# Kernel optimization log

Measured on AMD Instinct MI355X. Metric: run time of the kernel, lower is better.

Reference implementation:

```python
import jax, jax.numpy as jnp
import numpy as np
import math

H = 16
SEG = 128
DIL = 2


def hilbert_perm(M: int) -> jnp.ndarray:
    # Boustrophedon (snake) traversal of a ceil(sqrt(M)) grid, matching
    # create_hilbert_mapping_simple: skip linear positions >= M, keep first M.
    g = int(math.ceil(math.sqrt(M)))
    grid = np.arange(g * g).reshape(g, g)
    grid[1::2] = grid[1::2, ::-1]
    flat = grid.reshape(-1)
    flat = flat[flat < M][:M]
    return jnp.asarray(flat, dtype=jnp.int32)


def setup_inputs() -> dict:
    key = jax.random.key(0)
    kx, kq, ko = jax.random.split(key, 3)
    B, M, D = 4, 4096, 1024
    x = jax.random.normal(kx, (B, M, D), dtype=jnp.float32)
    # nn.Linear weights: [out_features, in_features], y = x @ W.T
    w_qkv = jax.random.normal(kq, (3 * D, D), dtype=jnp.float32) * (D ** -0.5)
    w_out = jax.random.normal(ko, (D, D), dtype=jnp.float32) * (D ** -0.5)
    return {"x": x, "w_qkv": w_qkv, "w_out": w_out}


def reference(x, w_qkv, w_out):
    B, M, Dm = x.shape
    hd = Dm // H
    scale = hd ** -0.5
    S = M // SEG  # number of segments (M chosen as a multiple of SEG)

    qkv = x @ w_qkv.T                              # [B, M, 3*Dm]
    qkv = qkv.reshape(B, M, 3, H, hd)
    q = qkv[:, :, 0].transpose(0, 2, 1, 3)         # [B, H, M, hd]
    k = qkv[:, :, 1].transpose(0, 2, 1, 3)
    v = qkv[:, :, 2].transpose(0, 2, 1, 3)

    perm = hilbert_perm(M)
    qh = q[:, :, perm]                             # Hilbert-reordered
    kh = k[:, :, perm]
    vh = v[:, :, perm]

    # segment-local dilated attention: each query attends to keys at
    # positions seg_start + j*DIL within its own segment
    qh = qh.reshape(B, H, S, SEG, hd)
    kd = kh.reshape(B, H, S, SEG, hd)[:, :, :, ::DIL]   # [B,H,S,SEG//DIL,hd]
    vd = vh.reshape(B, H, S, SEG, hd)[:, :, :, ::DIL]

    scores = jnp.einsum('bhsqd,bhskd->bhsqk', qh * scale, kd)
    attn = jax.nn.softmax(scores, axis=-1)
    o = jnp.einsum('bhsqk,bhskd->bhsqd', attn, vd)       # [B,H,S,SEG,hd]
    o = o.reshape(B, H, M, hd).transpose(0, 2, 1, 3).reshape(B, M, Dm)
    return o @ w_out.T
```

## Files before the change

### kernel.cpp

```cpp
#include <hip/hip_runtime.h>


typedef _Float16 f16x8 __attribute__((ext_vector_type(8)));
typedef _Float16 f16x4 __attribute__((ext_vector_type(4)));
typedef float f32x4 __attribute__((ext_vector_type(4)));

__device__ __forceinline__ int hperm(int i) {
  int r = i >> 6, c = i & 63;
  return (r << 6) | ((r & 1) ? (63 - c) : c);
}

__device__ __forceinline__ int arow_gather(int mp) {
  int b = mp >> 11, i = mp & 2047;
  int s = i >> 6, j = i & 63;
  return b * 4096 + hperm(s * 128 + 2 * j);
}

__device__ __forceinline__ void gload_lds16(const _Float16* g, _Float16* l) {
  __builtin_amdgcn_global_load_lds(
      (const __attribute__((address_space(1))) void*)g,
      (__attribute__((address_space(3))) void*)l, 16, 0, 0);
}

__global__ __launch_bounds__(256) void cast_all(
    const float* __restrict__ x, _Float16* __restrict__ xh,
    const float* __restrict__ wq, _Float16* __restrict__ wqh,
    const float* __restrict__ wo, _Float16* __restrict__ woh) {
  int i = blockIdx.x * 256 + threadIdx.x;
  const float* s;
  _Float16* d;
  int j;
  if (i < 4194304) {
    s = x; d = xh; j = i;
  } else if (i < 4194304 + 786432) {
    s = wq; d = wqh; j = i - 4194304;
  } else {
    s = wo; d = woh; j = i - (4194304 + 786432);
  }
  float4 v = ((const float4*)s)[j];
  f16x4 o;
  o[0] = (_Float16)v.x;
  o[1] = (_Float16)v.y;
  o[2] = (_Float16)v.z;
  o[3] = (_Float16)v.w;
  *(f16x4*)&d[(size_t)j * 4] = o;
}


#define BAR __builtin_amdgcn_s_barrier()
#define LGKM0                                          \
  do {                                                 \
    asm volatile("s_waitcnt lgkmcnt(0)" ::: "memory"); \
    __builtin_amdgcn_sched_barrier(0);                 \
  } while (0)
#define VM4 asm volatile("s_waitcnt vmcnt(4)" ::: "memory")
#define VM0 asm volatile("s_waitcnt vmcnt(0)" ::: "memory")

#define STG(mat, kt, h, buf)                                               \
  do {                                                                     \
    const _Float16* g0 = ((mat) ? gpB : gpA)[(h)*2] + (size_t)(kt)*64;     \
    const _Float16* g1 = ((mat) ? gpB : gpA)[(h)*2 + 1] + (size_t)(kt)*64; \
    _Float16* d_ = &lds[buf][mat][h][t * 8];                               \
    gload_lds16(g0, d_);                                                   \
    gload_lds16(g1, d_ + 4096);                                            \
  } while (0)

#define LDA_(buf, mh)                                             \
  _Pragma("unroll") for (int m = 0; m < 4; m++) {                 \
    a[0][m] = *(const f16x8*)(aB[buf][0] + (mh)*4096 + m * 1024); \
    a[1][m] = *(const f16x8*)(aB[buf][1] + (mh)*4096 + m * 1024); \
  }

#define LDB_(buf, nh)                                                   \
  _Pragma("unroll") for (int nf = 0; nf < 2; nf++) {                    \
    b[nh][0][nf] = *(const f16x8*)(bB[buf][0] + (nh)*2048 + nf * 1024); \
    b[nh][1][nf] = *(const f16x8*)(bB[buf][1] + (nh)*2048 + nf * 1024); \
  }

#define MM_(mh, nh)                                                        \
  __builtin_amdgcn_s_setprio(1);                                           \
  _Pragma("unroll") for (int m = 0; m < 4; m++)                            \
      _Pragma("unroll") for (int nf = 0; nf < 2; nf++)                     \
          _Pragma("unroll") for (int ks = 0; ks < 2; ks++) acc[(mh)*4 + m] \
              [(nh)*2 + nf] = __builtin_amdgcn_mfma_f32_16x16x32_f16(      \
                  a[ks][m], b[nh][ks][nf], acc[(mh)*4 + m][(nh)*2 + nf],   \
                  0, 0, 0);                                                \
  __builtin_amdgcn_s_setprio(0);

template <typename OutT>
__device__ __forceinline__ void gemm_body(
    const _Float16* const* gpA, const _Float16* const* gpB,
    OutT* __restrict__ C, int N, size_t arow0, size_t brow0,
    _Float16 (&lds)[2][2][2][8192]) {
  const int t = threadIdx.x;
  const int lane = t & 63, wave = t >> 6;
  const int wm = wave >> 2, wn = wave & 3;
  const int lr = lane & 15, lg = lane >> 4;

  const int cx0 = (lg * 8) ^ ((lr & 7) << 3);
  const int cx1 = cx0 ^ 32;
  const _Float16* aB[2][2];
  const _Float16* bB[2][2];
#pragma unroll
  for (int bf = 0; bf < 2; bf++) {
    aB[bf][0] = &lds[bf][0][wm][lr * 64 + cx0];
    aB[bf][1] = &lds[bf][0][wm][lr * 64 + cx1];
    bB[bf][0] = &lds[bf][1][wn >> 1][(wn & 1) * 4096 + lr * 64 + cx0];
    bB[bf][1] = &lds[bf][1][wn >> 1][(wn & 1) * 4096 + lr * 64 + cx1];
  }

  f32x4 acc[8][4] = {};
  f16x8 a[2][4], b[2][2][2];

  STG(0, 0, 0, 0);
  STG(0, 0, 1, 0);
  STG(1, 0, 0, 0);
  STG(1, 0, 1, 0);
  STG(1, 1, 0, 1);
  STG(1, 1, 1, 1);
  VM4;
  BAR;

  for (int i = 0; i < 7; i++) {
    const int k1 = 2 * i + 1, k2 = 2 * i + 2, k3 = 2 * i + 3;
    LDA_(0, 0); LDB_(0, 0); STG(0, k1, 0, 1);      BAR; LGKM0; MM_(0, 0);
    LDB_(0, 1);             STG(0, k1, 1, 1);      BAR; LGKM0; MM_(0, 1);
    LDA_(0, 1);             STG(1, k2, 0, 0);      BAR; LGKM0; MM_(1, 1);
                            STG(1, k2, 1, 0); VM4; BAR; LGKM0; MM_(1, 0);
    LDA_(1, 0); LDB_(1, 0); STG(0, k2, 0, 0);      BAR; LGKM0; MM_(0, 0);
    LDB_(1, 1);             STG(0, k2, 1, 0);      BAR; LGKM0; MM_(0, 1);
    LDA_(1, 1);             STG(1, k3, 0, 1);      BAR; LGKM0; MM_(1, 1);
                            STG(1, k3, 1, 1); VM4; BAR; LGKM0; MM_(1, 0);
  }

  {
    LDA_(0, 0); LDB_(0, 0); STG(0, 15, 0, 1);      BAR; LGKM0; MM_(0, 0);
    LDB_(0, 1);             STG(0, 15, 1, 1);      BAR; LGKM0; MM_(0, 1);
    LDA_(0, 1);                                    BAR; LGKM0; MM_(1, 1);
                                              VM0; BAR; LGKM0; MM_(1, 0);
    LDA_(1, 0); LDB_(1, 0);                        BAR; LGKM0; MM_(0, 0);
    LDB_(1, 1);                                    BAR; LGKM0; MM_(0, 1);
    LDA_(1, 1);                                    BAR; LGKM0; MM_(1, 1);
                                                        LGKM0; MM_(1, 0);
  }

#pragma unroll
  for (int mf = 0; mf < 8; mf++) {
    size_t row0 = arow0 + wm * 128 + mf * 16 + lg * 4;
#pragma unroll
    for (int nf = 0; nf < 4; nf++) {
      size_t col = brow0 + wn * 64 + nf * 16 + lr;
#pragma unroll
      for (int j = 0; j < 4; j++)
        C[(row0 + j) * N + col] = (OutT)acc[mf][nf][j];
    }
  }
}

__global__ __launch_bounds__(512, 2) void gemm_qkv8(
    const _Float16* __restrict__ xh, const _Float16* __restrict__ wqh,
    _Float16* __restrict__ qh, _Float16* __restrict__ kvh) {
  __shared__ _Float16 lds[2][2][2][8192];
  const int t = threadIdx.x;
  const int id = blockIdx.x;
  const int sw = (id & 7) * (gridDim.x >> 3) + (id >> 3);
  const bool iskv = sw >= 256;
  const int wid = iskv ? sw - 256 : sw;
  const int N = iskv ? 2048 : 1024;
  const int bn = iskv ? (wid & 7) : (wid & 3);
  const int bm = iskv ? (wid >> 3) : (wid >> 2);
  const _Float16* Bw = wqh + (iskv ? (size_t)1048576 : 0);
  _Float16* C = iskv ? kvh : qh;

  const int sgrow = t >> 3;
  const int sgcol = ((t & 7) * 8) ^ ((sgrow & 7) << 3);
  const _Float16* gpA[4];
  const _Float16* gpB[4];
#pragma unroll
  for (int r = 0; r < 4; r++) {
    int mr = bm * 256 + 64 * r + sgrow;
    int ar = iskv ? arow_gather(mr) : mr;
    gpA[r] = xh + (size_t)ar * 1024 + sgcol;
    gpB[r] = Bw + ((size_t)bn * 256 + 64 * r + sgrow) * 1024 + sgcol;
  }
  gemm_body<_Float16>(gpA, gpB, C, N, (size_t)bm * 256, (size_t)bn * 256, lds);
}

__global__ __launch_bounds__(512, 2) void gemm_out8(
    const _Float16* __restrict__ atth, const _Float16* __restrict__ woh,
    float* __restrict__ out) {
  __shared__ _Float16 lds[2][2][2][8192];
  const int t = threadIdx.x;
  const int id = blockIdx.x;
  const int sw = (id & 7) * (gridDim.x >> 3) + (id >> 3);
  const int bn = sw & 3, bm = sw >> 2;

  const int sgrow = t >> 3;
  const int sgcol = ((t & 7) * 8) ^ ((sgrow & 7) << 3);
  const _Float16* gpA[4];
  const _Float16* gpB[4];
#pragma unroll
  for (int r = 0; r < 4; r++) {
    gpA[r] = atth + ((size_t)bm * 256 + 64 * r + sgrow) * 1024 + sgcol;
    gpB[r] = woh + ((size_t)bn * 256 + 64 * r + sgrow) * 1024 + sgcol;
  }
  gemm_body<float>(gpA, gpB, out, 1024, (size_t)bm * 256, (size_t)bn * 256,
                   lds);
}

#define STRD 72

__global__ __launch_bounds__(256) void hilbert_attn(
    const _Float16* __restrict__ qh, const _Float16* __restrict__ kvh,
    _Float16* __restrict__ aout) {
  __shared__ _Float16 Qs[128 * STRD];
  __shared__ _Float16 Ks[64 * STRD];
  __shared__ _Float16 Vt[64 * STRD];
  __shared__ _Float16 Ps[128 * STRD];
  const int blk = blockIdx.x;
  const int s = blk & 31, h = (blk >> 5) & 15, b = blk >> 9;
  const int t = threadIdx.x, lane = t & 63, wave = t >> 6;
  const int lr = lane & 15, lg = lane >> 4, lk = lg * 8;
  const int col = (t & 7) * 8, rr = t >> 3;
  const size_t kvb = ((size_t)b * 2048 + s * 64) * 2048;

#pragma unroll
  for (int i = 0; i < 4; i++) {
    int m = i * 32 + rr;
    int p = b * 4096 + hperm(s * 128 + m);
    *(f16x8*)&Qs[m * STRD + col] =
        *(const f16x8*)&qh[(size_t)p * 1024 + h * 64 + col];
  }
#pragma unroll
  for (int i = 0; i < 2; i++) {
    int j = i * 32 + rr;
    *(f16x8*)&Ks[j * STRD + col] =
        *(const f16x8*)&kvh[kvb + (size_t)j * 2048 + h * 64 + col];
    f16x8 vv =
        *(const f16x8*)&kvh[kvb + (size_t)j * 2048 + 1024 + h * 64 + col];
#pragma unroll
    for (int e = 0; e < 8; e++) Vt[(col + e) * STRD + j] = vv[e];
  }
  __syncthreads();

  f32x4 accs[2][4] = {};
#pragma unroll
  for (int kk = 0; kk < 2; kk++) {
    f16x8 aa[2], bb[4];
#pragma unroll
    for (int m = 0; m < 2; m++)
      aa[m] = *(const f16x8*)&Qs[(wave * 32 + m * 16 + lr) * STRD + kk * 32 + lk];
#pragma unroll
    for (int n = 0; n < 4; n++)
      bb[n] = *(const f16x8*)&Ks[(n * 16 + lr) * STRD + kk * 32 + lk];
#pragma unroll
    for (int m = 0; m < 2; m++)
#pragma unroll
      for (int n = 0; n < 4; n++)
        accs[m][n] =
            __builtin_amdgcn_mfma_f32_16x16x32_f16(aa[m], bb[n], accs[m][n], 0, 0, 0);
  }

#pragma unroll
  for (int m = 0; m < 2; m++) {
#pragma unroll
    for (int j = 0; j < 4; j++) {
      float sc0 = accs[m][0][j] * 0.125f;
      float sc1 = accs[m][1][j] * 0.125f;
      float sc2 = accs[m][2][j] * 0.125f;
      float sc3 = accs[m][3][j] * 0.125f;
      float mx = fmaxf(fmaxf(sc0, sc1), fmaxf(sc2, sc3));
#pragma unroll
      for (int d = 1; d < 16; d <<= 1) mx = fmaxf(mx, __shfl_xor(mx, d, 16));
      float e0 = __expf(sc0 - mx), e1 = __expf(sc1 - mx);
      float e2 = __expf(sc2 - mx), e3 = __expf(sc3 - mx);
      float sum = (e0 + e1) + (e2 + e3);
#pragma unroll
      for (int d = 1; d < 16; d <<= 1) sum += __shfl_xor(sum, d, 16);
      float inv = 1.0f / sum;
      int row = wave * 32 + m * 16 + lg * 4 + j;
      Ps[row * STRD + 0 * 16 + lr] = (_Float16)(e0 * inv);
      Ps[row * STRD + 1 * 16 + lr] = (_Float16)(e1 * inv);
      Ps[row * STRD + 2 * 16 + lr] = (_Float16)(e2 * inv);
      Ps[row * STRD + 3 * 16 + lr] = (_Float16)(e3 * inv);
    }
  }
  __syncthreads();

  f32x4 acco[2][4] = {};
#pragma unroll
  for (int kk = 0; kk < 2; kk++) {
    f16x8 aa[2], bb[4];
#pragma unroll
    for (int m = 0; m < 2; m++)
      aa[m] = *(const f16x8*)&Ps[(wave * 32 + m * 16 + lr) * STRD + kk * 32 + lk];
#pragma unroll
    for (int n = 0; n < 4; n++)
      bb[n] = *(const f16x8*)&Vt[(n * 16 + lr) * STRD + kk * 32 + lk];
#pragma unroll
    for (int m = 0; m < 2; m++)
#pragma unroll
      for (int n = 0; n < 4; n++)
        acco[m][n] =
            __builtin_amdgcn_mfma_f32_16x16x32_f16(aa[m], bb[n], acco[m][n], 0, 0, 0);
  }

  const size_t orow0 = (size_t)b * 4096 + s * 128;
#pragma unroll
  for (int m = 0; m < 2; m++) {
#pragma unroll
    for (int n = 0; n < 4; n++) {
#pragma unroll
      for (int j = 0; j < 4; j++) {
        size_t row = orow0 + wave * 32 + m * 16 + lg * 4 + j;
        aout[row * 1024 + h * 64 + n * 16 + lr] = (_Float16)acco[m][n][j];
      }
    }
  }
}

extern "C" void kernel_launch(void* const* d_in, const int* in_sizes, int n_in,
                              void* d_out, int out_size, void* d_ws, size_t ws_size,
                              hipStream_t stream) {
  const float* x = (const float*)d_in[0];
  const float* w_qkv = (const float*)d_in[1];
  const float* w_out = (const float*)d_in[2];
  float* out = (float*)d_out;
  char* ws = (char*)d_ws;

  _Float16* xh = (_Float16*)(ws + 0);
  _Float16* wqh = (_Float16*)(ws + (size_t)33554432);
  _Float16* woh = (_Float16*)(ws + (size_t)39845888);
  _Float16* qh = (_Float16*)(ws + (size_t)41943040);
  _Float16* kvh = (_Float16*)(ws + (size_t)75497472);
  _Float16* atth = (_Float16*)(ws + (size_t)109051904);

  cast_all<<<20480, 256, 0, stream>>>(x, xh, w_qkv, wqh, w_out, woh);

  gemm_qkv8<<<512, 512, 0, stream>>>(xh, wqh, qh, kvh);
  hilbert_attn<<<2048, 256, 0, stream>>>(qh, kvh, atth);
  gemm_out8<<<256, 512, 0, stream>>>(atth, woh, out);
}
```

Baseline: 158.4 us.

## Restructure GEMM main loop with 4x2 wave layout and register double-buffered A fragments

```diff
diff --git a/kernel.cpp b/kernel.cpp
--- a/kernel.cpp
+++ b/kernel.cpp
@@ -9,13 +9,11 @@
   int r = i >> 6, c = i & 63;
   return (r << 6) | ((r & 1) ? (63 - c) : c);
 }
-
 __device__ __forceinline__ int arow_gather(int mp) {
   int b = mp >> 11, i = mp & 2047;
   int s = i >> 6, j = i & 63;
   return b * 4096 + hperm(s * 128 + 2 * j);
 }
-
 __device__ __forceinline__ void gload_lds16(const _Float16* g, _Float16* l) {
   __builtin_amdgcn_global_load_lds(
       (const __attribute__((address_space(1))) void*)g,
@@ -26,141 +24,151 @@
     const float* __restrict__ x, _Float16* __restrict__ xh,
     const float* __restrict__ wq, _Float16* __restrict__ wqh,
     const float* __restrict__ wo, _Float16* __restrict__ woh) {
-  int i = blockIdx.x * 256 + threadIdx.x;
-  const float* s;
-  _Float16* d;
-  int j;
-  if (i < 4194304) {
-    s = x; d = xh; j = i;
-  } else if (i < 4194304 + 786432) {
-    s = wq; d = wqh; j = i - 4194304;
-  } else {
-    s = wo; d = woh; j = i - (4194304 + 786432);
-  }
-  float4 v = ((const float4*)s)[j];
-  f16x4 o;
-  o[0] = (_Float16)v.x;
-  o[1] = (_Float16)v.y;
-  o[2] = (_Float16)v.z;
-  o[3] = (_Float16)v.w;
-  *(f16x4*)&d[(size_t)j * 4] = o;
-}
-
+  for (int i = blockIdx.x * 256 + threadIdx.x; i < 5242880; i += 256 * 2048) {
+    const float* s;
+    _Float16* d;
+    int j;
+    if (i < 4194304) {
+      s = x; d = xh; j = i;
+    } else if (i < 4980736) {
+      s = wq; d = wqh; j = i - 4194304;
+    } else {
+      s = wo; d = woh; j = i - 4980736;
+    }
+    float4 v = ((const float4*)s)[j];
+    f16x4 o;
+    o[0] = (_Float16)v.x;
+    o[1] = (_Float16)v.y;
+    o[2] = (_Float16)v.z;
+    o[3] = (_Float16)v.w;
+    *(f16x4*)&d[(size_t)j * 4] = o;
+  }
+}
 
 #define BAR __builtin_amdgcn_s_barrier()
-#define LGKM0                                          \
-  do {                                                 \
-    asm volatile("s_waitcnt lgkmcnt(0)" ::: "memory"); \
-    __builtin_amdgcn_sched_barrier(0);                 \
+#define SB0 __builtin_amdgcn_sched_barrier(0)
+#define LGKM_(n)                                                  \
+  do {                                                            \
+    asm volatile("s_waitcnt lgkmcnt(" #n ")" ::: "memory");       \
+    SB0;                                                          \
   } while (0)
 #define VM4 asm volatile("s_waitcnt vmcnt(4)" ::: "memory")
+#define VM2 asm volatile("s_waitcnt vmcnt(2)" ::: "memory")
 #define VM0 asm volatile("s_waitcnt vmcnt(0)" ::: "memory")
-
-#define STG(mat, kt, h, buf)                                               \
-  do {                                                                     \
-    const _Float16* g0 = ((mat) ? gpB : gpA)[(h)*2] + (size_t)(kt)*64;     \
-    const _Float16* g1 = ((mat) ? gpB : gpA)[(h)*2 + 1] + (size_t)(kt)*64; \
-    _Float16* d_ = &lds[buf][mat][h][t * 8];                               \
-    gload_lds16(g0, d_);                                                   \
-    gload_lds16(g1, d_ + 4096);                                            \
+#define VMX
+
+#define RDA(dst, bi, ks)                                       \
+  _Pragma("unroll") for (int m = 0; m < 4; m++) dst[ks][m] =   \
+      *(const f16x8*)(aRd[bi][ks] + m * 1024);
+#define RDB(dst, bi, q)                                                     \
+  _Pragma("unroll") for (int ks = 0; ks < 2; ks++)                          \
+      _Pragma("unroll") for (int nf = 0; nf < 2; nf++) dst[ks][nf] =        \
+          *(const f16x8*)(bRd[bi][ks] + (q)*2048 + nf * 1024);
+
+#define SA(kt, buf, h)                                                        \
+  do {                                                                        \
+    gload_lds16(Ab + aOff[(h)*2] + (kt)*64, &lds[buf][0][(h)*8192 + t8]);     \
+    gload_lds16(Ab + aOff[(h)*2 + 1] + (kt)*64,                               \
+                &lds[buf][0][(h)*8192 + 4096 + t8]);                          \
   } while (0)
-
-#define LDA_(buf, mh)                                             \
-  _Pragma("unroll") for (int m = 0; m < 4; m++) {                 \
-    a[0][m] = *(const f16x8*)(aB[buf][0] + (mh)*4096 + m * 1024); \
-    a[1][m] = *(const f16x8*)(aB[buf][1] + (mh)*4096 + m * 1024); \
-  }
-
-#define LDB_(buf, nh)                                                   \
-  _Pragma("unroll") for (int nf = 0; nf < 2; nf++) {                    \
-    b[nh][0][nf] = *(const f16x8*)(bB[buf][0] + (nh)*2048 + nf * 1024); \
-    b[nh][1][nf] = *(const f16x8*)(bB[buf][1] + (nh)*2048 + nf * 1024); \
-  }
-
-#define MM_(mh, nh)                                                        \
-  __builtin_amdgcn_s_setprio(1);                                           \
-  _Pragma("unroll") for (int m = 0; m < 4; m++)                            \
-      _Pragma("unroll") for (int nf = 0; nf < 2; nf++)                     \
-          _Pragma("unroll") for (int ks = 0; ks < 2; ks++) acc[(mh)*4 + m] \
-              [(nh)*2 + nf] = __builtin_amdgcn_mfma_f32_16x16x32_f16(      \
-                  a[ks][m], b[nh][ks][nf], acc[(mh)*4 + m][(nh)*2 + nf],   \
-                  0, 0, 0);                                                \
+#define SBt(kt, buf, h)                                                       \
+  do {                                                                        \
+    gload_lds16(Bb + bOff[(h)*2] + (kt)*64, &lds[buf][1][(h)*8192 + t8]);     \
+    gload_lds16(Bb + bOff[(h)*2 + 1] + (kt)*64,                               \
+                &lds[buf][1][(h)*8192 + 4096 + t8]);                          \
+  } while (0)
+
+#define MMQ(AC, BS, q)                                                      \
+  __builtin_amdgcn_s_setprio(1);                                            \
+  _Pragma("unroll") for (int m = 0; m < 4; m++)                             \
+      _Pragma("unroll") for (int nf = 0; nf < 2; nf++)                      \
+          _Pragma("unroll") for (int ks = 0; ks < 2; ks++) acc[m][2 * (q) + \
+                                                               nf] =        \
+              __builtin_amdgcn_mfma_f32_16x16x32_f16(                       \
+                  AC[ks][m], BS[ks][nf], acc[m][2 * (q) + nf], 0, 0, 0);    \
   __builtin_amdgcn_s_setprio(0);
+
+#define KT(P, T, RD_A, S1, S2, S3, VQ2, VQ3, RD_B0, AN, AC, LGA, LGB3) \
+  do {                                                                 \
+                                                               \
+    if (RD_A) { RDA(AN, (P) ^ 1, 0); }                                 \
+    RDB(bS1, (P), 1);                                                  \
+    if (S1) { SBt((T) + 1, (P) ^ 1, 1); }                              \
+    BAR; LGKM_(LGA); MMQ(AC, bS0, 0);                                  \
+                                                               \
+    if (RD_A) { RDA(AN, (P) ^ 1, 1); }                                 \
+    RDB(bS0, (P), 2);                                                  \
+    if (S2) { SA((T) + 2, (P), 0); }                                   \
+    BAR; LGKM_(LGA); MMQ(AC, bS1, 1);                                  \
+                                                               \
+    RDB(bS1, (P), 3);                                                  \
+    if (S2) { SA((T) + 2, (P), 1); }                                   \
+    VQ2; BAR; LGKM_(4); MMQ(AC, bS0, 2);                               \
+                                                               \
+    if (RD_B0) { RDB(bS0, (P) ^ 1, 0); }                               \
+    if (S3) { SBt((T) + 2, (P), 0); }                                  \
+    VQ3; BAR; LGKM_(LGB3); MMQ(AC, bS1, 3);                            \
+  } while (0)
 
 template <typename OutT>
 __device__ __forceinline__ void gemm_body(
-    const _Float16* const* gpA, const _Float16* const* gpB,
-    OutT* __restrict__ C, int N, size_t arow0, size_t brow0,
-    _Float16 (&lds)[2][2][2][8192]) {
+    const _Float16* __restrict__ Ab, const _Float16* __restrict__ Bb,
+    const unsigned* aOff, const unsigned* bOff, OutT* __restrict__ C, int N,
+    size_t arow0, size_t bcol0, _Float16 (&lds)[2][2][16384]) {
   const int t = threadIdx.x;
   const int lane = t & 63, wave = t >> 6;
-  const int wm = wave >> 2, wn = wave & 3;
+  const int wm = wave >> 1, wn = wave & 1;
   const int lr = lane & 15, lg = lane >> 4;
+  const int t8 = t * 8;
 
   const int cx0 = (lg * 8) ^ ((lr & 7) << 3);
   const int cx1 = cx0 ^ 32;
-  const _Float16* aB[2][2];
-  const _Float16* bB[2][2];
+  const _Float16* aRd[2][2];
+  const _Float16* bRd[2][2];
 #pragma unroll
   for (int bf = 0; bf < 2; bf++) {
-    aB[bf][0] = &lds[bf][0][wm][lr * 64 + cx0];
-    aB[bf][1] = &lds[bf][0][wm][lr * 64 + cx1];
-    bB[bf][0] = &lds[bf][1][wn >> 1][(wn & 1) * 4096 + lr * 64 + cx0];
-    bB[bf][1] = &lds[bf][1][wn >> 1][(wn & 1) * 4096 + lr * 64 + cx1];
-  }
-
-  f32x4 acc[8][4] = {};
-  f16x8 a[2][4], b[2][2][2];
-
-  STG(0, 0, 0, 0);
-  STG(0, 0, 1, 0);
-  STG(1, 0, 0, 0);
-  STG(1, 0, 1, 0);
-  STG(1, 1, 0, 1);
-  STG(1, 1, 1, 1);
+    aRd[bf][0] = &lds[bf][0][(wm * 64 + lr) * 64 + cx0];
+    aRd[bf][1] = &lds[bf][0][(wm * 64 + lr) * 64 + cx1];
+    bRd[bf][0] = &lds[bf][1][(wn * 128 + lr) * 64 + cx0];
+    bRd[bf][1] = &lds[bf][1][(wn * 128 + lr) * 64 + cx1];
+  }
+
+  f32x4 acc[4][8] = {};
+  f16x8 aEv[2][4], aOd[2][4], bS0[2][2], bS1[2][2];
+
+  SA(0, 0, 0); SA(0, 0, 1); SBt(0, 0, 0); SBt(0, 0, 1);
+  SA(1, 1, 0); SA(1, 1, 1);
   VM4;
   BAR;
+  RDA(aEv, 0, 0); RDA(aEv, 0, 1); RDB(bS0, 0, 0);
+  SBt(1, 1, 0);
+  VM2;
+  BAR;
 
   for (int i = 0; i < 7; i++) {
-    const int k1 = 2 * i + 1, k2 = 2 * i + 2, k3 = 2 * i + 3;
-    LDA_(0, 0); LDB_(0, 0); STG(0, k1, 0, 1);      BAR; LGKM0; MM_(0, 0);
-    LDB_(0, 1);             STG(0, k1, 1, 1);      BAR; LGKM0; MM_(0, 1);
-    LDA_(0, 1);             STG(1, k2, 0, 0);      BAR; LGKM0; MM_(1, 1);
-                            STG(1, k2, 1, 0); VM4; BAR; LGKM0; MM_(1, 0);
-    LDA_(1, 0); LDB_(1, 0); STG(0, k2, 0, 0);      BAR; LGKM0; MM_(0, 0);
-    LDB_(1, 1);             STG(0, k2, 1, 0);      BAR; LGKM0; MM_(0, 1);
-    LDA_(1, 1);             STG(1, k3, 0, 1);      BAR; LGKM0; MM_(1, 1);
-                            STG(1, k3, 1, 1); VM4; BAR; LGKM0; MM_(1, 0);
-  }
-
-  {
-    LDA_(0, 0); LDB_(0, 0); STG(0, 15, 0, 1);      BAR; LGKM0; MM_(0, 0);
-    LDB_(0, 1);             STG(0, 15, 1, 1);      BAR; LGKM0; MM_(0, 1);
-    LDA_(0, 1);                                    BAR; LGKM0; MM_(1, 1);
-                                              VM0; BAR; LGKM0; MM_(1, 0);
-    LDA_(1, 0); LDB_(1, 0);                        BAR; LGKM0; MM_(0, 0);
-    LDB_(1, 1);                                    BAR; LGKM0; MM_(0, 1);
-    LDA_(1, 1);                                    BAR; LGKM0; MM_(1, 1);
-                                                        LGKM0; MM_(1, 0);
-  }
-
-#pragma unroll
-  for (int mf = 0; mf < 8; mf++) {
-    size_t row0 = arow0 + wm * 128 + mf * 16 + lg * 4;
-#pragma unroll
-    for (int nf = 0; nf < 4; nf++) {
-      size_t col = brow0 + wn * 64 + nf * 16 + lr;
+    KT(0, 2 * i,     1, 1, 1, 1, VM4, VM2, 1, aOd, aEv, 8, 4);
+    KT(1, 2 * i + 1, 1, 1, 1, 1, VM4, VM2, 1, aEv, aOd, 8, 4);
+  }
+  KT(0, 14, 1, 1, 0, 0, VM0, VMX, 1, aOd, aEv, 8, 4);
+  KT(1, 15, 0, 0, 0, 0, VMX, VMX, 0, aEv, aOd, 4, 0);
+
+#pragma unroll
+  for (int m = 0; m < 4; m++) {
+    size_t row0 = arow0 + wm * 64 + m * 16 + lg * 4;
+#pragma unroll
+    for (int n = 0; n < 8; n++) {
+      size_t col = bcol0 + wn * 128 + (n >> 1) * 32 + (n & 1) * 16 + lr;
 #pragma unroll
       for (int j = 0; j < 4; j++)
-        C[(row0 + j) * N + col] = (OutT)acc[mf][nf][j];
+        C[(row0 + j) * N + col] = (OutT)acc[m][n][j];
     }
   }
 }
 
-__global__ __launch_bounds__(512, 2) void gemm_qkv8(
+__global__ __launch_bounds__(512, 2) void gemm_qkv(
     const _Float16* __restrict__ xh, const _Float16* __restrict__ wqh,
     _Float16* __restrict__ qh, _Float16* __restrict__ kvh) {
-  __shared__ _Float16 lds[2][2][2][8192];
+  __shared__ _Float16 lds[2][2][16384];
   const int t = threadIdx.x;
   const int id = blockIdx.x;
   const int sw = (id & 7) * (gridDim.x >> 3) + (id >> 3);
@@ -169,27 +177,27 @@
   const int N = iskv ? 2048 : 1024;
   const int bn = iskv ? (wid & 7) : (wid & 3);
   const int bm = iskv ? (wid >> 3) : (wid >> 2);
-  const _Float16* Bw = wqh + (iskv ? (size_t)1048576 : 0);
+  const _Float16* Bb = wqh + (iskv ? (size_t)1048576 : 0);
   _Float16* C = iskv ? kvh : qh;
 
   const int sgrow = t >> 3;
   const int sgcol = ((t & 7) * 8) ^ ((sgrow & 7) << 3);
-  const _Float16* gpA[4];
-  const _Float16* gpB[4];
+  unsigned aOff[4], bOff[4];
 #pragma unroll
   for (int r = 0; r < 4; r++) {
     int mr = bm * 256 + 64 * r + sgrow;
     int ar = iskv ? arow_gather(mr) : mr;
-    gpA[r] = xh + (size_t)ar * 1024 + sgcol;
-    gpB[r] = Bw + ((size_t)bn * 256 + 64 * r + sgrow) * 1024 + sgcol;
-  }
-  gemm_body<_Float16>(gpA, gpB, C, N, (size_t)bm * 256, (size_t)bn * 256, lds);
-}
-
-__global__ __launch_bounds__(512, 2) void gemm_out8(
+    aOff[r] = (unsigned)ar * 1024u + (unsigned)sgcol;
+    bOff[r] = ((unsigned)(bn * 256 + 64 * r + sgrow)) * 1024u + (unsigned)sgcol;
+  }
+  gemm_body<_Float16>(xh, Bb, aOff, bOff, C, N, (size_t)bm * 256,
+                      (size_t)bn * 256, lds);
+}
+
+__global__ __launch_bounds__(512, 2) void gemm_out(
     const _Float16* __restrict__ atth, const _Float16* __restrict__ woh,
     float* __restrict__ out) {
-  __shared__ _Float16 lds[2][2][2][8192];
+  __shared__ _Float16 lds[2][2][16384];
   const int t = threadIdx.x;
   const int id = blockIdx.x;
   const int sw = (id & 7) * (gridDim.x >> 3) + (id >> 3);
@@ -197,15 +205,14 @@
 
   const int sgrow = t >> 3;
   const int sgcol = ((t & 7) * 8) ^ ((sgrow & 7) << 3);
-  const _Float16* gpA[4];
-  const _Float16* gpB[4];
+  unsigned aOff[4], bOff[4];
 #pragma unroll
   for (int r = 0; r < 4; r++) {
-    gpA[r] = atth + ((size_t)bm * 256 + 64 * r + sgrow) * 1024 + sgcol;
-    gpB[r] = woh + ((size_t)bn * 256 + 64 * r + sgrow) * 1024 + sgcol;
-  }
-  gemm_body<float>(gpA, gpB, out, 1024, (size_t)bm * 256, (size_t)bn * 256,
-                   lds);
+    aOff[r] = ((unsigned)(bm * 256 + 64 * r + sgrow)) * 1024u + (unsigned)sgcol;
+    bOff[r] = ((unsigned)(bn * 256 + 64 * r + sgrow)) * 1024u + (unsigned)sgcol;
+  }
+  gemm_body<float>(atth, woh, aOff, bOff, out, 1024, (size_t)bm * 256,
+                   (size_t)bn * 256, lds);
 }
 
 #define STRD 72
@@ -335,9 +342,9 @@
   _Float16* kvh = (_Float16*)(ws + (size_t)75497472);
   _Float16* atth = (_Float16*)(ws + (size_t)109051904);
 
-  cast_all<<<20480, 256, 0, stream>>>(x, xh, w_qkv, wqh, w_out, woh);
-
-  gemm_qkv8<<<512, 512, 0, stream>>>(xh, wqh, qh, kvh);
+  cast_all<<<2048, 256, 0, stream>>>(x, xh, w_qkv, wqh, w_out, woh);
+
+  gemm_qkv<<<512, 512, 0, stream>>>(xh, wqh, qh, kvh);
   hilbert_attn<<<2048, 256, 0, stream>>>(qh, kvh, atth);
-  gemm_out8<<<256, 512, 0, stream>>>(atth, woh, out);
-}
+  gemm_out<<<256, 512, 0, stream>>>(atth, woh, out);
+}
```

Measured after the change: 173.2 us. +9.4%, slower.
